# Optimization experiments

Measured on AMD Instinct MI355X. Metric: run time of the kernel, lower is better.

Reference implementation:

```python
import jax, jax.numpy as jnp
import numpy as np

HIDDEN_DIM = 256
N = 8192


def setup_inputs() -> dict:
    key = jax.random.key(0)
    k1, k2, k3, k4 = jax.random.split(key, 4)
    img = jax.random.normal(k1, (N, HIDDEN_DIM), dtype=jnp.float32)
    text = jax.random.normal(k2, (N, HIDDEN_DIM), dtype=jnp.float32)
    # nn.Linear(hidden_dim, hidden_dim, bias=False) weights, shape [out, in]
    scale = 1.0 / np.sqrt(HIDDEN_DIM)
    Wq = jax.random.uniform(k3, (HIDDEN_DIM, HIDDEN_DIM), dtype=jnp.float32, minval=-scale, maxval=scale)
    Wk = jax.random.uniform(k4, (HIDDEN_DIM, HIDDEN_DIM), dtype=jnp.float32, minval=-scale, maxval=scale)
    return {"img": img, "text": text, "Wq": Wq, "Wk": Wk}


def reference(img, text, Wq, Wk):
    d = img.shape[-1]
    norm_fact = 1.0 / jnp.sqrt(jnp.asarray(d, dtype=img.dtype))
    Q = img @ Wq.T                       # [N, D]
    K = text @ Wk.T                      # [N, D]
    scores = Q @ K.T                     # [N, N]
    # softmax over dim=1 (keys), then scaled by 1/sqrt(D)
    attn = jax.nn.softmax(scores, axis=1) * norm_fact
    out_img = attn @ img                 # [N, D]
    out_text = attn @ text               # [N, D]
    return (out_img, out_text)
```

## Files before the change

### kernel.cpp

```cpp
#include <hip/hip_runtime.h>

typedef unsigned short ushort_t;
typedef unsigned int uint_t;
typedef __attribute__((ext_vector_type(8))) short short8;
typedef __attribute__((ext_vector_type(8))) _Float16 half8;
typedef __attribute__((ext_vector_type(4))) float float4v;

#define MFMA_BF16(a, b, c) __builtin_amdgcn_mfma_f32_16x16x32_bf16((a), (b), (c), 0, 0, 0)
#define MFMA_F16(a, b, c) __builtin_amdgcn_mfma_f32_16x16x32_f16((a), (b), (c), 0, 0, 0)

#define NQ 8192
#define DIM 256
#define DV 512

__device__ __forceinline__ ushort_t f2bf(float x) {
  union { float f; uint_t u; } v; v.f = x;
  return (ushort_t)((v.u + 0x7fffu + ((v.u >> 16) & 1u)) >> 16);
}
__device__ __forceinline__ float bf2f(ushort_t b) {
  union { uint_t u; float f; } v; v.u = ((uint_t)b) << 16;
  return v.f;
}

__device__ __forceinline__ half8 cvt8h(const float* p) {
  float4v a = *(const float4v*)p;
  float4v b = *(const float4v*)(p + 4);
  half8 r;
  r[0] = (_Float16)a[0]; r[1] = (_Float16)a[1];
  r[2] = (_Float16)a[2]; r[3] = (_Float16)a[3];
  r[4] = (_Float16)b[0]; r[5] = (_Float16)b[1];
  r[6] = (_Float16)b[2]; r[7] = (_Float16)b[3];
  return r;
}

__device__ __forceinline__ half8 as_h8(short8 s) {
  union { short8 s; half8 h; } u; u.s = s; return u.h;
}

__device__ __forceinline__ void load_lds_16(const void* g, void* l) {
  __builtin_amdgcn_global_load_lds(
      (const __attribute__((address_space(1))) uint_t*)g,
      (__attribute__((address_space(3))) uint_t*)l, 16, 0, 0);
}

__global__ __launch_bounds__(256, 2) void proj_kernel(
    const float* __restrict__ img, const float* __restrict__ text,
    const float* __restrict__ Wq, const float* __restrict__ Wk,
    _Float16* __restrict__ Qh, _Float16* __restrict__ Kh) {
  const int lane = threadIdx.x & 63;
  const int wv = threadIdx.x >> 6;
  const int l16 = lane & 15;
  const int quad = lane >> 4;
  const float* A = blockIdx.z ? text : img;
  const float* W = blockIdx.z ? Wk : Wq;
  _Float16* C = blockIdx.z ? Kh : Qh;
  const int row = blockIdx.x * 64 + wv * 16 + l16;
  const int colbase = blockIdx.y * 64;

  float4v acc[4];
#pragma unroll
  for (int c = 0; c < 4; ++c) acc[c] = (float4v){0.f, 0.f, 0.f, 0.f};

#pragma unroll
  for (int f = 0; f < 8; ++f) {
    const int k0 = f * 32 + quad * 8;
    half8 af = cvt8h(A + (size_t)row * DIM + k0);
#pragma unroll
    for (int c = 0; c < 4; ++c) {
      half8 bfr = cvt8h(W + (size_t)(colbase + c * 16 + l16) * DIM + k0);
      acc[c] = MFMA_F16(af, bfr, acc[c]);
    }
  }
  const int rbase = blockIdx.x * 64 + wv * 16 + quad * 4;
#pragma unroll
  for (int c = 0; c < 4; ++c)
#pragma unroll
    for (int r = 0; r < 4; ++r)
      C[(size_t)(rbase + r) * DIM + colbase + c * 16 + l16] = (_Float16)acc[c][r];
}

__global__ __launch_bounds__(256) void make_vt_kernel(
    const float* __restrict__ img, const float* __restrict__ text,
    ushort_t* __restrict__ Vt) {
  __shared__ float tile[64][65];
  const int n0 = blockIdx.x * 64;
  const int c0 = blockIdx.y * 64;
  const float* src = (c0 < 256) ? img : text;
  const int cc0 = (c0 < 256) ? c0 : (c0 - 256);
  const int tid = threadIdx.x;

#pragma unroll
  for (int i = 0; i < 4; ++i) {
    const int r = i * 16 + (tid >> 4);
    const int c = (tid & 15) * 4;
    *(float4v*)&tile[r][c] = *(const float4v*)(src + (size_t)(n0 + r) * DIM + cc0 + c);
  }
  __syncthreads();
  const int c = tid >> 2;
  const int seg = tid & 3;
  ushort_t tmp[16];
#pragma unroll
  for (int t = 0; t < 16; ++t) tmp[t] = f2bf(tile[seg * 16 + t][c]);
  ushort_t* dst = Vt + (size_t)(c0 + c) * NQ + n0 + seg * 16;
  *(short8*)dst = *(short8*)&tmp[0];
  *(short8*)(dst + 8) = *(short8*)&tmp[8];
}

__global__ __launch_bounds__(256, 2) void attn_kernel(
    const _Float16* __restrict__ Qh, const _Float16* __restrict__ Kh,
    const ushort_t* __restrict__ Vt, float* __restrict__ pacc,
    float* __restrict__ pdenom, int kps) {
  __shared__ __align__(16) ushort_t ldsK[32 * DIM];
  __shared__ __align__(16) ushort_t ldsV[DV * 32];
  __shared__ __align__(16) ushort_t ldsP[4 * 16 * 40];

  const int tid = threadIdx.x;
  const int lane = tid & 63;
  const int wv = tid >> 6;
  const int l16 = lane & 15;
  const int quad = lane >> 4;
  const int qtile = blockIdx.x;
  const int split = blockIdx.y;
  const int kbeg = split * kps;

  short8 qf[8];
  {
    const _Float16* qptr = Qh + (size_t)(qtile * 64 + wv * 16 + l16) * DIM;
#pragma unroll
    for (int f = 0; f < 8; ++f)
      qf[f] = *(const short8*)(qptr + f * 32 + quad * 8);
  }

  float4v acc[32];
#pragma unroll
  for (int t = 0; t < 32; ++t) acc[t] = (float4v){0.f, 0.f, 0.f, 0.f};
  float dacc[4] = {0.f, 0.f, 0.f, 0.f};

  ushort_t* pb = ldsP + wv * 640;

  const int ntiles = kps >> 5;
  for (int it = 0; it < ntiles; ++it) {
    const int k0 = kbeg + it * 32;
    __syncthreads();
#pragma unroll
    for (int i = 0; i < 4; ++i) {
      const int chunk = i * 256 + tid;
      const int n = chunk >> 5;
      const int cs = (chunk & 31) ^ (n & 7);
      load_lds_16(Kh + (size_t)(k0 + n) * DIM + cs * 8,
                  (char*)ldsK + (i * 256 + wv * 64) * 16);
    }
#pragma unroll
    for (int i = 0; i < 8; ++i) {
      const int chunk = i * 256 + tid;
      const int vrow = chunk >> 2;
      const int off = (chunk & 3) * 8;
      load_lds_16(Vt + (size_t)vrow * NQ + k0 + off,
                  (char*)ldsV + (i * 256 + wv * 64) * 16);
    }
    __syncthreads();

    float4v s0 = (float4v){0.f, 0.f, 0.f, 0.f};
    float4v s1 = (float4v){0.f, 0.f, 0.f, 0.f};
    const int sw = l16 & 7;
#pragma unroll
    for (int f = 0; f < 8; ++f) {
      const int cs = ((f * 4 + quad) ^ sw) * 8;
      short8 kb0 = *(const short8*)(ldsK + l16 * DIM + cs);
      short8 kb1 = *(const short8*)(ldsK + (l16 + 16) * DIM + cs);
      s0 = MFMA_F16(as_h8(qf[f]), as_h8(kb0), s0);
      s1 = MFMA_F16(as_h8(qf[f]), as_h8(kb1), s1);
    }

    ushort_t pb0[4], pb1[4];
    float p0[4], p1[4];
#pragma unroll
    for (int r = 0; r < 4; ++r) {
      pb0[r] = f2bf(__expf(s0[r]));
      pb1[r] = f2bf(__expf(s1[r]));
      p0[r] = bf2f(pb0[r]);
      p1[r] = bf2f(pb1[r]);
    }
#pragma unroll
    for (int r = 0; r < 4; ++r) {
      float t = p0[r] + p1[r];
      t += __shfl_xor(t, 1);
      t += __shfl_xor(t, 2);
      t += __shfl_xor(t, 4);
      t += __shfl_xor(t, 8);
      dacc[r] += t;
    }
#pragma unroll
    for (int r = 0; r < 4; ++r) {
      pb[(quad * 4 + r) * 40 + l16] = pb0[r];
      pb[(quad * 4 + r) * 40 + l16 + 16] = pb1[r];
    }
    __threadfence_block();
    short8 pa = *(const short8*)(pb + l16 * 40 + quad * 8);

#pragma unroll
    for (int c = 0; c < 32; ++c) {
      short8 vb = *(const short8*)(ldsV + (c * 16 + l16) * 32 + quad * 8);
      acc[c] = MFMA_BF16(pa, vb, acc[c]);
    }
  }

  float* pout = pacc + (size_t)split * ((size_t)NQ * DV);
  const int rowbase = qtile * 64 + wv * 16 + quad * 4;
#pragma unroll
  for (int c = 0; c < 32; ++c)
#pragma unroll
    for (int r = 0; r < 4; ++r)
      pout[(size_t)(rowbase + r) * DV + c * 16 + l16] = acc[c][r];
  if (l16 == 0) {
#pragma unroll
    for (int r = 0; r < 4; ++r)
      pdenom[split * NQ + rowbase + r] = dacc[r];
  }
}

__global__ __launch_bounds__(256) void combine_kernel(
    const float* __restrict__ pacc, const float* __restrict__ pdenom,
    float* __restrict__ out, int ks) {
  const int idx = blockIdx.x * 256 + threadIdx.x;
  const int n = idx >> 7;
  const int c4 = (idx & 127) << 2;
  float4v s = (float4v){0.f, 0.f, 0.f, 0.f};
  float d = 0.f;
  for (int sp = 0; sp < ks; ++sp) {
    s += *(const float4v*)(pacc + (size_t)sp * ((size_t)NQ * DV) + (size_t)n * DV + c4);
    d += pdenom[sp * NQ + n];
  }
  const float scale = 1.0f / (16.0f * d);
  s *= scale;
  float* dst = (c4 < 256) ? (out + (size_t)n * DIM + c4)
                          : (out + (size_t)NQ * DIM + (size_t)n * DIM + (c4 - 256));
  *(float4v*)dst = s;
}

extern "C" void kernel_launch(void* const* d_in, const int* in_sizes, int n_in,
                              void* d_out, int out_size, void* d_ws, size_t ws_size,
                              hipStream_t stream) {
  const float* img = (const float*)d_in[0];
  const float* text = (const float*)d_in[1];
  const float* Wq = (const float*)d_in[2];
  const float* Wk = (const float*)d_in[3];
  float* out = (float*)d_out;
  char* ws = (char*)d_ws;

  _Float16* Qh = (_Float16*)ws;
  _Float16* Kh = (_Float16*)(ws + ((size_t)4 << 20));
  ushort_t* Vt = (ushort_t*)(ws + ((size_t)8 << 20));
  const size_t accsz = (size_t)NQ * DV * sizeof(float);
  const size_t base = (size_t)16 << 20;

  int ks = 4;
  if (ws_size < base + 4 * (accsz + NQ * sizeof(float))) ks = 2;
  if (ws_size < base + 2 * (accsz + NQ * sizeof(float))) ks = 1;
  float* pacc = (float*)(ws + base);
  float* pdenom = (float*)(ws + base + (size_t)ks * accsz);

  hipLaunchKernelGGL(proj_kernel, dim3(128, 4, 2), dim3(256), 0, stream,
                     img, text, Wq, Wk, Qh, Kh);
  hipLaunchKernelGGL(make_vt_kernel, dim3(128, 8), dim3(256), 0, stream,
                     img, text, Vt);
  hipLaunchKernelGGL(attn_kernel, dim3(128, ks), dim3(256), 0, stream,
                     Qh, Kh, Vt, pacc, pdenom, NQ / ks);
  hipLaunchKernelGGL(combine_kernel, dim3((NQ * DV / 4) / 256), dim3(256), 0, stream,
                     pacc, pdenom, out, ks);
}
```

Measured before the change: 284.8 us.

## Split PV matmul across waves by output columns with shared P tile

Before, each wave computed the P·V product for its own 16 query rows across all 512 value columns, so every wave read the whole V tile from LDS. Now all four waves write their P rows into one shared 64x32 LDS tile, and each wave computes all 64 rows for its own 128-column slice of V. Each V fragment is therefore reused across four MFMAs, which cuts LDS traffic for V. XOR swizzles on the V and P LDS layouts are added to avoid bank conflicts. The cost is an extra block-wide __syncthreads per key tile, which replaces the per-wave fence.

```diff
diff --git a/kernel.cpp b/kernel.cpp
--- a/kernel.cpp
+++ b/kernel.cpp
@@ -112,7 +112,7 @@
     float* __restrict__ pdenom, int kps) {
   __shared__ __align__(16) ushort_t ldsK[32 * DIM];
   __shared__ __align__(16) ushort_t ldsV[DV * 32];
-  __shared__ __align__(16) ushort_t ldsP[4 * 16 * 40];
+  __shared__ __align__(16) ushort_t ldsP[64 * 32];
 
   const int tid = threadIdx.x;
   const int lane = tid & 63;
@@ -122,6 +122,7 @@
   const int qtile = blockIdx.x;
   const int split = blockIdx.y;
   const int kbeg = split * kps;
+  const int sw2 = (l16 >> 1) & 3;
 
   short8 qf[8];
   {
@@ -131,12 +132,12 @@
       qf[f] = *(const short8*)(qptr + f * 32 + quad * 8);
   }
 
-  float4v acc[32];
-#pragma unroll
-  for (int t = 0; t < 32; ++t) acc[t] = (float4v){0.f, 0.f, 0.f, 0.f};
+  float4v acc[4][8];
+#pragma unroll
+  for (int m = 0; m < 4; ++m)
+#pragma unroll
+    for (int c = 0; c < 8; ++c) acc[m][c] = (float4v){0.f, 0.f, 0.f, 0.f};
   float dacc[4] = {0.f, 0.f, 0.f, 0.f};
-
-  ushort_t* pb = ldsP + wv * 640;
 
   const int ntiles = kps >> 5;
   for (int it = 0; it < ntiles; ++it) {
@@ -154,18 +155,18 @@
     for (int i = 0; i < 8; ++i) {
       const int chunk = i * 256 + tid;
       const int vrow = chunk >> 2;
-      const int off = (chunk & 3) * 8;
-      load_lds_16(Vt + (size_t)vrow * NQ + k0 + off,
+      const int dc = (chunk & 3) ^ ((vrow >> 1) & 3);
+      load_lds_16(Vt + (size_t)vrow * NQ + k0 + dc * 8,
                   (char*)ldsV + (i * 256 + wv * 64) * 16);
     }
     __syncthreads();
 
     float4v s0 = (float4v){0.f, 0.f, 0.f, 0.f};
     float4v s1 = (float4v){0.f, 0.f, 0.f, 0.f};
-    const int sw = l16 & 7;
+    const int swk = l16 & 7;
 #pragma unroll
     for (int f = 0; f < 8; ++f) {
-      const int cs = ((f * 4 + quad) ^ sw) * 8;
+      const int cs = ((f * 4 + quad) ^ swk) * 8;
       short8 kb0 = *(const short8*)(ldsK + l16 * DIM + cs);
       short8 kb1 = *(const short8*)(ldsK + (l16 + 16) * DIM + cs);
       s0 = MFMA_F16(as_h8(qf[f]), as_h8(kb0), s0);
@@ -173,46 +174,61 @@
     }
 
     ushort_t pb0[4], pb1[4];
-    float p0[4], p1[4];
 #pragma unroll
     for (int r = 0; r < 4; ++r) {
       pb0[r] = f2bf(__expf(s0[r]));
       pb1[r] = f2bf(__expf(s1[r]));
-      p0[r] = bf2f(pb0[r]);
-      p1[r] = bf2f(pb1[r]);
     }
 #pragma unroll
     for (int r = 0; r < 4; ++r) {
-      float t = p0[r] + p1[r];
+      float t = bf2f(pb0[r]) + bf2f(pb1[r]);
       t += __shfl_xor(t, 1);
       t += __shfl_xor(t, 2);
       t += __shfl_xor(t, 4);
       t += __shfl_xor(t, 8);
       dacc[r] += t;
     }
-#pragma unroll
-    for (int r = 0; r < 4; ++r) {
-      pb[(quad * 4 + r) * 40 + l16] = pb0[r];
-      pb[(quad * 4 + r) * 40 + l16 + 16] = pb1[r];
-    }
-    __threadfence_block();
-    short8 pa = *(const short8*)(pb + l16 * 40 + quad * 8);
-
-#pragma unroll
-    for (int c = 0; c < 32; ++c) {
-      short8 vb = *(const short8*)(ldsV + (c * 16 + l16) * 32 + quad * 8);
-      acc[c] = MFMA_BF16(pa, vb, acc[c]);
+    {
+      const int swr = ((wv * 16 + quad * 4) >> 1) & 3;
+#pragma unroll
+      for (int r = 0; r < 4; ++r) {
+        const int rb = wv * 16 + quad * 4 + r;
+        const int swp = (rb >> 1) & 3;
+        ldsP[rb * 32 + ((l16 >> 3) ^ swp) * 8 + (l16 & 7)] = pb0[r];
+        ldsP[rb * 32 + ((2 + (l16 >> 3)) ^ swp) * 8 + (l16 & 7)] = pb1[r];
+      }
+      (void)swr;
+    }
+    __syncthreads();
+
+    short8 pa[4];
+#pragma unroll
+    for (int m = 0; m < 4; ++m)
+      pa[m] = *(const short8*)(ldsP + (m * 16 + l16) * 32 + (quad ^ sw2) * 8);
+#pragma unroll
+    for (int c = 0; c < 8; ++c) {
+      const int vcol = (wv * 8 + c) * 16 + l16;
+      short8 vb = *(const short8*)(ldsV + vcol * 32 + (quad ^ sw2) * 8);
+#pragma unroll
+      for (int m = 0; m < 4; ++m)
+        acc[m][c] = MFMA_BF16(pa[m], vb, acc[m][c]);
     }
   }
 
   float* pout = pacc + (size_t)split * ((size_t)NQ * DV);
-  const int rowbase = qtile * 64 + wv * 16 + quad * 4;
-#pragma unroll
-  for (int c = 0; c < 32; ++c)
-#pragma unroll
-    for (int r = 0; r < 4; ++r)
-      pout[(size_t)(rowbase + r) * DV + c * 16 + l16] = acc[c][r];
+#pragma unroll
+  for (int m = 0; m < 4; ++m) {
+    const int rowbase = qtile * 64 + m * 16 + quad * 4;
+#pragma unroll
+    for (int c = 0; c < 8; ++c) {
+      const int col = (wv * 8 + c) * 16 + l16;
+#pragma unroll
+      for (int r = 0; r < 4; ++r)
+        pout[(size_t)(rowbase + r) * DV + col] = acc[m][c][r];
+    }
+  }
   if (l16 == 0) {
+    const int rowbase = qtile * 64 + wv * 16 + quad * 4;
 #pragma unroll
     for (int r = 0; r < 4; ++r)
       pdenom[split * NQ + rowbase + r] = dacc[r];
```

After: 275.4 us. -3.3%, faster.
